# Kernel optimization log

Measured on AMD Instinct MI355X. Metric: run time of the kernel, lower is better.

Reference implementation:

```python
import jax, jax.numpy as jnp
import numpy as np

N_EMBD = 1024
N_HEADS = 16
HEAD_DIM = N_EMBD // N_HEADS


def setup_inputs() -> dict:
    key = jax.random.key(0)
    k0, k1, k2, k3, k4 = jax.random.split(key, 5)
    scale = 1.0 / np.sqrt(N_EMBD)
    x = jax.random.normal(k0, (2, 2048, N_EMBD), dtype=jnp.float32)
    # nn.Linear(n_embd, 3*n_embd): weight [3d, d], bias [3d]
    w_qkv = jax.random.normal(k1, (3 * N_EMBD, N_EMBD), dtype=jnp.float32) * scale
    b_qkv = jax.random.normal(k2, (3 * N_EMBD,), dtype=jnp.float32) * scale
    w_proj = jax.random.normal(k3, (N_EMBD, N_EMBD), dtype=jnp.float32) * scale
    b_proj = jax.random.normal(k4, (N_EMBD,), dtype=jnp.float32) * scale
    return {"x": x, "w_qkv": w_qkv, "b_qkv": b_qkv, "w_proj": w_proj, "b_proj": b_proj}


def reference(x, w_qkv, b_qkv, w_proj, b_proj):
    b, l, d = x.shape
    h, f = N_HEADS, HEAD_DIM
    qkv = x @ w_qkv.T + b_qkv                      # [b, l, 3d]
    # rearrange 'b l (c h f) -> c b h l f'
    qkv = qkv.reshape(b, l, 3, h, f)
    q = jnp.transpose(qkv[:, :, 0], (0, 2, 1, 3))  # [b, h, l, f]
    k = jnp.transpose(qkv[:, :, 1], (0, 2, 1, 3))
    v = jnp.transpose(qkv[:, :, 2], (0, 2, 1, 3))
    scores = jnp.einsum('bhqf,bhkf->bhqk', q, k) / jnp.sqrt(jnp.float32(f))
    att = jax.nn.softmax(scores, axis=-1)          # [b, h, l, l]
    y = jnp.einsum('bhqk,bhkf->bhqf', att, v)      # [b, h, l, f]
    y = jnp.transpose(y, (0, 2, 1, 3)).reshape(b, l, d)  # 'b h l f -> b l (h f)'
    return y @ w_proj.T + b_proj
```

## Files before the change

### kernel.cpp

```cpp
#include <hip/hip_runtime.h>
#include <hip/hip_bf16.h>
#include <stdint.h>


typedef unsigned short u16;
typedef __attribute__((ext_vector_type(8))) short short8;
typedef __attribute__((ext_vector_type(4))) float f32x4;

#define MFMA16(a, b, c) __builtin_amdgcn_mfma_f32_16x16x32_bf16((a), (b), (c), 0, 0, 0)

__device__ __forceinline__ u16 f2bf(float x) {
  union { float f; uint32_t u; } v; v.f = x;
  uint32_t r = v.u + 0x7FFFu + ((v.u >> 16) & 1u);
  return (u16)(r >> 16);
}

__device__ __forceinline__ float fexp2(float x) {
#if __has_builtin(__builtin_amdgcn_exp2f)
  return __builtin_amdgcn_exp2f(x);
#else
  return exp2f(x);
#endif
}

__device__ __forceinline__ uint32_t pkbf(float lo, float hi) {
  uint32_t a = __builtin_bit_cast(uint32_t, lo) + 0x8000u;
  uint32_t b = __builtin_bit_cast(uint32_t, hi) + 0x8000u;
  return __builtin_amdgcn_perm(b, a, 0x07060302u);
}

__device__ __forceinline__ void gload16(const void* g, void* l) {
  __builtin_amdgcn_global_load_lds((const __attribute__((address_space(1))) void*)g,
                                   (__attribute__((address_space(3))) void*)l, 16, 0, 0);
}

__global__ __launch_bounds__(256) void cvt_all(const float* __restrict__ x,
                                               const float* __restrict__ wq,
                                               const float* __restrict__ wp,
                                               u16* __restrict__ xb,
                                               u16* __restrict__ wqb,
                                               u16* __restrict__ wpb) {
  int i = blockIdx.x * 256 + threadIdx.x;
  const float* s; u16* d; int off;
  if (i < 1048576) { s = x; d = xb; off = i; }
  else if (i < 1835008) { s = wq; d = wqb; off = i - 1048576; }
  else { s = wp; d = wpb; off = i - 1835008; }
  float4 f = reinterpret_cast<const float4*>(s)[off];
  ushort4 o;
  o.x = f2bf(f.x); o.y = f2bf(f.y); o.z = f2bf(f.z); o.w = f2bf(f.w);
  reinterpret_cast<ushort4*>(d)[off] = o;
}

template <int EPI>
__global__ __launch_bounds__(256) void gemm_bt(const u16* __restrict__ A,
                                               const u16* __restrict__ B,
                                               const float* __restrict__ bias,
                                               u16* __restrict__ outb,
                                               float* __restrict__ outf,
                                               int M, int N, int K) {
  __shared__ u16 sA[128 * 32];
  __shared__ u16 sB[128 * 32];
  const int tid = threadIdx.x;
  const int lane = tid & 63;
  const int wid = tid >> 6;
  const int bn = blockIdx.x, bm = blockIdx.y;
  const int row0 = bm * 128, col0 = bn * 128;
  const int wr = wid >> 1, wc = wid & 1;
  const int fr = lane & 15, fq = lane >> 4;

  f32x4 acc[4][4];
  #pragma unroll
  for (int m = 0; m < 4; m++)
    #pragma unroll
    for (int n = 0; n < 4; n++)
      #pragma unroll
      for (int j = 0; j < 4; j++) acc[m][n][j] = 0.f;

  const int e1 = tid * 8;
  const int e2 = e1 + 2048;
  const int r1 = e1 >> 5, c1 = e1 & 31;
  const int r2 = e2 >> 5;
  const u16* Ap1 = A + (size_t)(row0 + r1) * K + c1;
  const u16* Ap2 = A + (size_t)(row0 + r2) * K + c1;
  const u16* Bp1 = B + (size_t)(col0 + r1) * K + c1;
  const u16* Bp2 = B + (size_t)(col0 + r2) * K + c1;

  for (int k0 = 0; k0 < K; k0 += 32) {
    __syncthreads();
    gload16(Ap1 + k0, &sA[e1]);
    gload16(Ap2 + k0, &sA[e2]);
    gload16(Bp1 + k0, &sB[e1]);
    gload16(Bp2 + k0, &sB[e2]);
    __syncthreads();
    short8 a[4], b[4];
    #pragma unroll
    for (int m = 0; m < 4; m++)
      a[m] = *(const short8*)&sA[(wr * 64 + m * 16 + fr) * 32 + fq * 8];
    #pragma unroll
    for (int n = 0; n < 4; n++)
      b[n] = *(const short8*)&sB[(wc * 64 + n * 16 + fr) * 32 + fq * 8];
    #pragma unroll
    for (int m = 0; m < 4; m++)
      #pragma unroll
      for (int n = 0; n < 4; n++)
        acc[m][n] = MFMA16(a[m], b[n], acc[m][n]);
  }

  #pragma unroll
  for (int m = 0; m < 4; m++) {
    #pragma unroll
    for (int n = 0; n < 4; n++) {
      #pragma unroll
      for (int j = 0; j < 4; j++) {
        int r = row0 + wr * 64 + m * 16 + fq * 4 + j;
        int c = col0 + wc * 64 + n * 16 + fr;
        float v = acc[m][n][j] + bias[c];
        if (EPI == 0) {
          int cc = c >> 10, d = c & 1023, h = d >> 6, f = d & 63;
          int bb = r >> 11, ll = r & 2047;
          int bhh = bb * 16 + h;
          if (cc == 0) {
            outb[((size_t)bhh * 2048 + ll) * 64 + f] = f2bf(v * 0.18033688f);
          } else if (cc == 1) {
            outb[4194304u + ((size_t)bhh * 2048 + ll) * 64 + f] = f2bf(v);
          } else {
            outb[8388608u + ((size_t)bhh * 64 + f) * 2048 + ll] = f2bf(v);
          }
        } else {
          outf[(size_t)r * N + c] = v;
        }
      }
    }
  }
}

__global__ __launch_bounds__(256, 2) void attn_kernel(const u16* __restrict__ qg,
                                                      const u16* __restrict__ kg,
                                                      const u16* __restrict__ vtg,
                                                      u16* __restrict__ y) {
  __shared__ u16 sK[2][4096];
  __shared__ u16 sVt[2][4096];
  __shared__ u16 sP[4][2048];
  const int x = blockIdx.x;
  const int bh = (x & 7) * 4 + (x >> 7);
  const int qt = (x >> 3) & 15;
  const int tid = threadIdx.x, lane = tid & 63, wid = tid >> 6;
  const int fr = lane & 15, fq = lane >> 4;
  const size_t base = (size_t)bh * 131072;
  const u16* qp = qg + base;
  const u16* kp = kg + base;
  const u16* vp = vtg + base;
  const int qrow = qt * 128 + wid * 32;

  const int c2 = tid + 256;
  const int r1 = tid >> 3, r2 = c2 >> 3;
  const int sw1 = ((tid & 7) * 8) ^ ((r1 & 7) << 3);
  const int sw2 = ((c2 & 7) * 8) ^ ((r2 & 7) << 3);
  const int ko1 = r1 * 64 + sw1, ko2 = r2 * 64 + sw2;
  const int vo1 = r1 * 2048 + sw1, vo2 = r2 * 2048 + sw2;
  const int d1 = tid * 8, d2 = c2 * 8;

  short8 qf[2][2];
  #pragma unroll
  for (int mr = 0; mr < 2; mr++)
    #pragma unroll
    for (int hh = 0; hh < 2; hh++)
      qf[mr][hh] = *(const short8*)&qp[(size_t)(qrow + mr * 16 + fr) * 64 + hh * 32 + fq * 8];

  f32x4 o[2][4];
  float lp[2] = {0.f, 0.f};
  #pragma unroll
  for (int mr = 0; mr < 2; mr++)
    #pragma unroll
    for (int ct = 0; ct < 4; ct++)
      #pragma unroll
      for (int j = 0; j < 4; j++) o[mr][ct][j] = 0.f;

  const int swr = (fr & 7) << 3;

  gload16(kp + ko1, &sK[0][d1]);
  gload16(kp + ko2, &sK[0][d2]);
  gload16(vp + vo1, &sVt[0][d1]);
  gload16(vp + vo2, &sVt[0][d2]);

  int sel = 0;
  for (int t0 = 0; t0 < 2048; t0 += 64) {
    __syncthreads();
    if (t0 + 64 < 2048) {
      const int tn = t0 + 64;
      gload16(kp + (size_t)tn * 64 + ko1, &sK[sel ^ 1][d1]);
      gload16(kp + (size_t)tn * 64 + ko2, &sK[sel ^ 1][d2]);
      gload16(vp + tn + vo1, &sVt[sel ^ 1][d1]);
      gload16(vp + tn + vo2, &sVt[sel ^ 1][d2]);
    }
    const u16* Kt = sK[sel];
    const u16* Vt = sVt[sel];
    u16* P = sP[wid];

    f32x4 st[2][4];
    #pragma unroll
    for (int mr = 0; mr < 2; mr++)
      #pragma unroll
      for (int n = 0; n < 4; n++)
        #pragma unroll
        for (int j = 0; j < 4; j++) st[mr][n][j] = 0.f;
    #pragma unroll
    for (int n = 0; n < 4; n++) {
      short8 kb0 = *(const short8*)&Kt[(n * 16 + fr) * 64 + ((fq * 8) ^ swr)];
      short8 kb1 = *(const short8*)&Kt[(n * 16 + fr) * 64 + ((32 + fq * 8) ^ swr)];
      st[0][n] = MFMA16(kb0, qf[0][0], st[0][n]);
      st[0][n] = MFMA16(kb1, qf[0][1], st[0][n]);
      st[1][n] = MFMA16(kb0, qf[1][0], st[1][n]);
      st[1][n] = MFMA16(kb1, qf[1][1], st[1][n]);
    }

    #pragma unroll
    for (int mr = 0; mr < 2; mr++) {
      const int prow = (mr * 16 + fr) * 64;
      #pragma unroll
      for (int n = 0; n < 4; n++) {
        float p0 = fexp2(st[mr][n][0]);
        float p1 = fexp2(st[mr][n][1]);
        float p2 = fexp2(st[mr][n][2]);
        float p3 = fexp2(st[mr][n][3]);
        lp[mr] += (p0 + p1) + (p2 + p3);
        uint2 w;
        w.x = pkbf(p0, p1);
        w.y = pkbf(p2, p3);
        *(uint2*)&P[prow + ((n * 16 + fq * 4) ^ swr)] = w;
      }
    }

    short8 pa[2][2];
    #pragma unroll
    for (int mr = 0; mr < 2; mr++) {
      pa[mr][0] = *(const short8*)&P[(mr * 16 + fr) * 64 + ((fq * 8) ^ swr)];
      pa[mr][1] = *(const short8*)&P[(mr * 16 + fr) * 64 + ((32 + fq * 8) ^ swr)];
    }
    #pragma unroll
    for (int ct = 0; ct < 4; ct++) {
      short8 vb0 = *(const short8*)&Vt[(ct * 16 + fr) * 64 + ((fq * 8) ^ swr)];
      short8 vb1 = *(const short8*)&Vt[(ct * 16 + fr) * 64 + ((32 + fq * 8) ^ swr)];
      #pragma unroll
      for (int mr = 0; mr < 2; mr++) {
        o[mr][ct] = MFMA16(pa[mr][0], vb0, o[mr][ct]);
        o[mr][ct] = MFMA16(pa[mr][1], vb1, o[mr][ct]);
      }
    }
    sel ^= 1;
  }

  #pragma unroll
  for (int mr = 0; mr < 2; mr++) {
    lp[mr] += __shfl_xor(lp[mr], 16);
    lp[mr] += __shfl_xor(lp[mr], 32);
  }
  const int b = bh >> 4, h = bh & 15;
  #pragma unroll
  for (int mr = 0; mr < 2; mr++) {
    #pragma unroll
    for (int j = 0; j < 4; j++) {
      int r = qrow + mr * 16 + fq * 4 + j;
      float lq = __shfl(lp[mr], fq * 4 + j);
      float inv = 1.0f / lq;
      #pragma unroll
      for (int ct = 0; ct < 4; ct++) {
        y[((size_t)(b * 2048 + r)) * 1024 + h * 64 + ct * 16 + fr] = f2bf(o[mr][ct][j] * inv);
      }
    }
  }
}

extern "C" void kernel_launch(void* const* d_in, const int* in_sizes, int n_in,
                              void* d_out, int out_size, void* d_ws, size_t ws_size,
                              hipStream_t stream) {
  const float* x = (const float*)d_in[0];
  const float* w_qkv = (const float*)d_in[1];
  const float* b_qkv = (const float*)d_in[2];
  const float* w_proj = (const float*)d_in[3];
  const float* b_proj = (const float*)d_in[4];
  float* out = (float*)d_out;

  u16* ws = (u16*)d_ws;
  u16* xb = ws;
  u16* wq = xb + 4194304;
  u16* wp = wq + 3145728;
  u16* qb = wp + 1048576;
  u16* kb = qb + 4194304;
  u16* vb = kb + 4194304;
  u16* yb = vb + 4194304;

  cvt_all<<<8192, 256, 0, stream>>>(x, w_qkv, w_proj, xb, wq, wp);

  gemm_bt<0><<<dim3(24, 32), 256, 0, stream>>>(xb, wq, b_qkv, qb, nullptr, 4096, 3072, 1024);

  attn_kernel<<<512, 256, 0, stream>>>(qb, kb, vb, yb);

  gemm_bt<1><<<dim3(8, 32), 256, 0, stream>>>(yb, wp, b_proj, nullptr, out, 4096, 1024, 1024);
}
```

Baseline: 134.7 us.

## Rewrite attention with 32x32 MFMA and register-resident P; stage V-transpose epilogue via LDS

Result: slower. 147.1 us (+9.2%).

```diff
diff --git a/kernel.cpp b/kernel.cpp
--- a/kernel.cpp
+++ b/kernel.cpp
@@ -6,8 +6,11 @@
 typedef unsigned short u16;
 typedef __attribute__((ext_vector_type(8))) short short8;
 typedef __attribute__((ext_vector_type(4))) float f32x4;
+typedef __attribute__((ext_vector_type(16))) float f32x16;
+typedef __attribute__((ext_vector_type(4))) unsigned int u32x4;
 
 #define MFMA16(a, b, c) __builtin_amdgcn_mfma_f32_16x16x32_bf16((a), (b), (c), 0, 0, 0)
+#define MFMA32(a, b, c) __builtin_amdgcn_mfma_f32_32x32x16_bf16((a), (b), (c), 0, 0, 0)
 
 __device__ __forceinline__ u16 f2bf(float x) {
   union { float f; uint32_t u; } v; v.f = x;
@@ -60,6 +63,7 @@
                                                int M, int N, int K) {
   __shared__ u16 sA[128 * 32];
   __shared__ u16 sB[128 * 32];
+  __shared__ u16 sC[EPI == 0 ? 128 * 128 : 8];
   const int tid = threadIdx.x;
   const int lane = tid & 63;
   const int wid = tid >> 6;
@@ -106,167 +110,193 @@
         acc[m][n] = MFMA16(a[m], b[n], acc[m][n]);
   }
 
-  #pragma unroll
-  for (int m = 0; m < 4; m++) {
-    #pragma unroll
-    for (int n = 0; n < 4; n++) {
-      #pragma unroll
-      for (int j = 0; j < 4; j++) {
-        int r = row0 + wr * 64 + m * 16 + fq * 4 + j;
-        int c = col0 + wc * 64 + n * 16 + fr;
-        float v = acc[m][n][j] + bias[c];
-        if (EPI == 0) {
-          int cc = c >> 10, d = c & 1023, h = d >> 6, f = d & 63;
-          int bb = r >> 11, ll = r & 2047;
-          int bhh = bb * 16 + h;
-          if (cc == 0) {
-            outb[((size_t)bhh * 2048 + ll) * 64 + f] = f2bf(v * 0.18033688f);
-          } else if (cc == 1) {
-            outb[4194304u + ((size_t)bhh * 2048 + ll) * 64 + f] = f2bf(v);
-          } else {
-            outb[8388608u + ((size_t)bhh * 64 + f) * 2048 + ll] = f2bf(v);
+  if (EPI == 0) {
+    if (bn < 16) {
+      #pragma unroll
+      for (int m = 0; m < 4; m++) {
+        #pragma unroll
+        for (int n = 0; n < 4; n++) {
+          #pragma unroll
+          for (int j = 0; j < 4; j++) {
+            int r = row0 + wr * 64 + m * 16 + fq * 4 + j;
+            int c = col0 + wc * 64 + n * 16 + fr;
+            float v = acc[m][n][j] + bias[c];
+            int d = c & 1023, h = d >> 6, f = d & 63;
+            int bb = r >> 11, ll = r & 2047;
+            int bhh = bb * 16 + h;
+            if (bn < 8) {
+              outb[((size_t)bhh * 2048 + ll) * 64 + f] = f2bf(v * 0.18033688f);
+            } else {
+              outb[4194304u + ((size_t)bhh * 2048 + ll) * 64 + f] = f2bf(v);
+            }
           }
-        } else {
-          outf[(size_t)r * N + c] = v;
         }
       }
-    }
-  }
-}
-
-__global__ __launch_bounds__(256, 2) void attn_kernel(const u16* __restrict__ qg,
+    } else {
+      #pragma unroll
+      for (int m = 0; m < 4; m++) {
+        #pragma unroll
+        for (int n = 0; n < 4; n++) {
+          int c_local = wc * 64 + n * 16 + fr;
+          int r_base = wr * 64 + m * 16 + fq * 4;
+          float bi = bias[col0 + c_local];
+          uint2 w;
+          w.x = pkbf(acc[m][n][0] + bi, acc[m][n][1] + bi);
+          w.y = pkbf(acc[m][n][2] + bi, acc[m][n][3] + bi);
+          *(uint2*)&sC[c_local * 128 + (r_base ^ ((c_local & 7) << 3))] = w;
+        }
+      }
+      __syncthreads();
+      const int h0 = (col0 - 2048) >> 6;
+      const int ll0 = row0 & 2047;
+      const int bb = row0 >> 11;
+      #pragma unroll
+      for (int it = 0; it < 8; it++) {
+        int chunk = tid + it * 256;
+        int row_c = chunk >> 4, off = chunk & 15;
+        short8 v = *(const short8*)&sC[row_c * 128 + ((off * 8) ^ ((row_c & 7) << 3))];
+        int h = h0 + (row_c >> 6), f = row_c & 63;
+        *(short8*)&outb[8388608u + ((size_t)((bb * 16 + h) * 64 + f)) * 2048 + ll0 + off * 8] = v;
+      }
+    }
+  } else {
+    #pragma unroll
+    for (int m = 0; m < 4; m++)
+      #pragma unroll
+      for (int n = 0; n < 4; n++)
+        #pragma unroll
+        for (int j = 0; j < 4; j++) {
+          int r = row0 + wr * 64 + m * 16 + fq * 4 + j;
+          int c = col0 + wc * 64 + n * 16 + fr;
+          outf[(size_t)r * N + c] = acc[m][n][j] + bias[c];
+        }
+  }
+}
+
+__device__ __forceinline__ void softpack(const f32x16& st, float& lp,
+                                         short8& paA, short8& paB) {
+  float e[16];
+  #pragma unroll
+  for (int r = 0; r < 16; r++) e[r] = fexp2(st[r]);
+  #pragma unroll
+  for (int r = 0; r < 16; r++) lp += e[r];
+  #pragma unroll
+  for (int cc = 0; cc < 2; cc++) {
+    uint32_t g0 = pkbf(e[8 * cc + 0], e[8 * cc + 1]);
+    uint32_t g1 = pkbf(e[8 * cc + 2], e[8 * cc + 3]);
+    uint32_t g2 = pkbf(e[8 * cc + 4], e[8 * cc + 5]);
+    uint32_t g3 = pkbf(e[8 * cc + 6], e[8 * cc + 7]);
+    asm volatile("v_permlane32_swap_b32 %0, %1" : "+v"(g0), "+v"(g2));
+    asm volatile("v_permlane32_swap_b32 %0, %1" : "+v"(g1), "+v"(g3));
+    u32x4 t;
+    t[0] = g0; t[1] = g1; t[2] = g2; t[3] = g3;
+    if (cc == 0) paA = __builtin_bit_cast(short8, t);
+    else paB = __builtin_bit_cast(short8, t);
+  }
+}
+
+__global__ __launch_bounds__(128, 2) void attn_kernel(const u16* __restrict__ qg,
                                                       const u16* __restrict__ kg,
                                                       const u16* __restrict__ vtg,
                                                       u16* __restrict__ y) {
   __shared__ u16 sK[2][4096];
   __shared__ u16 sVt[2][4096];
-  __shared__ u16 sP[4][2048];
+  __shared__ float sLv[2][32];
   const int x = blockIdx.x;
-  const int bh = (x & 7) * 4 + (x >> 7);
-  const int qt = (x >> 3) & 15;
-  const int tid = threadIdx.x, lane = tid & 63, wid = tid >> 6;
-  const int fr = lane & 15, fq = lane >> 4;
+  const int bh = (x & 7) * 4 + (x >> 8);
+  const int qt = (x >> 3) & 31;
+  const int tid = threadIdx.x, l = tid & 63, wid = tid >> 6;
+  const int col = l & 31, hi = l >> 5;
   const size_t base = (size_t)bh * 131072;
   const u16* qp = qg + base;
   const u16* kp = kg + base;
   const u16* vp = vtg + base;
-  const int qrow = qt * 128 + wid * 32;
-
-  const int c2 = tid + 256;
-  const int r1 = tid >> 3, r2 = c2 >> 3;
-  const int sw1 = ((tid & 7) * 8) ^ ((r1 & 7) << 3);
-  const int sw2 = ((c2 & 7) * 8) ^ ((r2 & 7) << 3);
-  const int ko1 = r1 * 64 + sw1, ko2 = r2 * 64 + sw2;
-  const int vo1 = r1 * 2048 + sw1, vo2 = r2 * 2048 + sw2;
-  const int d1 = tid * 8, d2 = c2 * 8;
-
-  short8 qf[2][2];
-  #pragma unroll
-  for (int mr = 0; mr < 2; mr++)
-    #pragma unroll
-    for (int hh = 0; hh < 2; hh++)
-      qf[mr][hh] = *(const short8*)&qp[(size_t)(qrow + mr * 16 + fr) * 64 + hh * 32 + fq * 8];
-
-  f32x4 o[2][4];
-  float lp[2] = {0.f, 0.f};
-  #pragma unroll
-  for (int mr = 0; mr < 2; mr++)
-    #pragma unroll
-    for (int ct = 0; ct < 4; ct++)
-      #pragma unroll
-      for (int j = 0; j < 4; j++) o[mr][ct][j] = 0.f;
-
-  const int swr = (fr & 7) << 3;
-
-  gload16(kp + ko1, &sK[0][d1]);
-  gload16(kp + ko2, &sK[0][d2]);
-  gload16(vp + vo1, &sVt[0][d1]);
-  gload16(vp + vo2, &sVt[0][d2]);
+  const int qrow = qt * 64 + wid * 32;
+
+  short8 qf[4];
+  #pragma unroll
+  for (int kk = 0; kk < 4; kk++)
+    qf[kk] = *(const short8*)&qp[(size_t)(qrow + col) * 64 + kk * 16 + hi * 8];
+
+  int koff[4], voff[4], dst[4];
+  #pragma unroll
+  for (int j = 0; j < 4; j++) {
+    int c = tid + j * 128;
+    int row = c >> 3, slot = c & 7;
+    int swc = (slot * 8) ^ ((row & 7) << 3);
+    koff[j] = row * 64 + swc;
+    voff[j] = row * 2048 + swc;
+    dst[j] = c * 8;
+  }
+
+  f32x16 o0, o1;
+  float lp = 0.f;
+  #pragma unroll
+  for (int r = 0; r < 16; r++) { o0[r] = 0.f; o1[r] = 0.f; }
+
+  const int rsw = (col & 7) << 3;
+
+  #pragma unroll
+  for (int j = 0; j < 4; j++) {
+    gload16(kp + koff[j], &sK[0][dst[j]]);
+    gload16(vp + voff[j], &sVt[0][dst[j]]);
+  }
 
   int sel = 0;
   for (int t0 = 0; t0 < 2048; t0 += 64) {
     __syncthreads();
     if (t0 + 64 < 2048) {
       const int tn = t0 + 64;
-      gload16(kp + (size_t)tn * 64 + ko1, &sK[sel ^ 1][d1]);
-      gload16(kp + (size_t)tn * 64 + ko2, &sK[sel ^ 1][d2]);
-      gload16(vp + tn + vo1, &sVt[sel ^ 1][d1]);
-      gload16(vp + tn + vo2, &sVt[sel ^ 1][d2]);
+      #pragma unroll
+      for (int j = 0; j < 4; j++) {
+        gload16(kp + (size_t)tn * 64 + koff[j], &sK[sel ^ 1][dst[j]]);
+        gload16(vp + tn + voff[j], &sVt[sel ^ 1][dst[j]]);
+      }
     }
     const u16* Kt = sK[sel];
     const u16* Vt = sVt[sel];
-    u16* P = sP[wid];
-
-    f32x4 st[2][4];
-    #pragma unroll
-    for (int mr = 0; mr < 2; mr++)
-      #pragma unroll
-      for (int n = 0; n < 4; n++)
-        #pragma unroll
-        for (int j = 0; j < 4; j++) st[mr][n][j] = 0.f;
-    #pragma unroll
-    for (int n = 0; n < 4; n++) {
-      short8 kb0 = *(const short8*)&Kt[(n * 16 + fr) * 64 + ((fq * 8) ^ swr)];
-      short8 kb1 = *(const short8*)&Kt[(n * 16 + fr) * 64 + ((32 + fq * 8) ^ swr)];
-      st[0][n] = MFMA16(kb0, qf[0][0], st[0][n]);
-      st[0][n] = MFMA16(kb1, qf[0][1], st[0][n]);
-      st[1][n] = MFMA16(kb0, qf[1][0], st[1][n]);
-      st[1][n] = MFMA16(kb1, qf[1][1], st[1][n]);
-    }
-
-    #pragma unroll
-    for (int mr = 0; mr < 2; mr++) {
-      const int prow = (mr * 16 + fr) * 64;
-      #pragma unroll
-      for (int n = 0; n < 4; n++) {
-        float p0 = fexp2(st[mr][n][0]);
-        float p1 = fexp2(st[mr][n][1]);
-        float p2 = fexp2(st[mr][n][2]);
-        float p3 = fexp2(st[mr][n][3]);
-        lp[mr] += (p0 + p1) + (p2 + p3);
-        uint2 w;
-        w.x = pkbf(p0, p1);
-        w.y = pkbf(p2, p3);
-        *(uint2*)&P[prow + ((n * 16 + fq * 4) ^ swr)] = w;
-      }
-    }
-
-    short8 pa[2][2];
-    #pragma unroll
-    for (int mr = 0; mr < 2; mr++) {
-      pa[mr][0] = *(const short8*)&P[(mr * 16 + fr) * 64 + ((fq * 8) ^ swr)];
-      pa[mr][1] = *(const short8*)&P[(mr * 16 + fr) * 64 + ((32 + fq * 8) ^ swr)];
-    }
-    #pragma unroll
-    for (int ct = 0; ct < 4; ct++) {
-      short8 vb0 = *(const short8*)&Vt[(ct * 16 + fr) * 64 + ((fq * 8) ^ swr)];
-      short8 vb1 = *(const short8*)&Vt[(ct * 16 + fr) * 64 + ((32 + fq * 8) ^ swr)];
-      #pragma unroll
-      for (int mr = 0; mr < 2; mr++) {
-        o[mr][ct] = MFMA16(pa[mr][0], vb0, o[mr][ct]);
-        o[mr][ct] = MFMA16(pa[mr][1], vb1, o[mr][ct]);
-      }
-    }
+
+    f32x16 st0, st1;
+    #pragma unroll
+    for (int r = 0; r < 16; r++) { st0[r] = 0.f; st1[r] = 0.f; }
+    __builtin_amdgcn_s_setprio(1);
+    #pragma unroll
+    for (int kk = 0; kk < 4; kk++) {
+      short8 kb0 = *(const short8*)&Kt[(col) * 64 + ((kk * 16 + hi * 8) ^ rsw)];
+      short8 kb1 = *(const short8*)&Kt[(32 + col) * 64 + ((kk * 16 + hi * 8) ^ rsw)];
+      st0 = MFMA32(kb0, qf[kk], st0);
+      st1 = MFMA32(kb1, qf[kk], st1);
+    }
+    __builtin_amdgcn_s_setprio(0);
+
+    short8 pa[4];
+    softpack(st0, lp, pa[0], pa[1]);
+    softpack(st1, lp, pa[2], pa[3]);
+
+    __builtin_amdgcn_s_setprio(1);
+    #pragma unroll
+    for (int c = 0; c < 4; c++) {
+      short8 vb0 = *(const short8*)&Vt[(col) * 64 + ((c * 16 + hi * 8) ^ rsw)];
+      short8 vb1 = *(const short8*)&Vt[(32 + col) * 64 + ((c * 16 + hi * 8) ^ rsw)];
+      o0 = MFMA32(pa[c], vb0, o0);
+      o1 = MFMA32(pa[c], vb1, o1);
+    }
+    __builtin_amdgcn_s_setprio(0);
     sel ^= 1;
   }
 
-  #pragma unroll
-  for (int mr = 0; mr < 2; mr++) {
-    lp[mr] += __shfl_xor(lp[mr], 16);
-    lp[mr] += __shfl_xor(lp[mr], 32);
-  }
-  const int b = bh >> 4, h = bh & 15;
-  #pragma unroll
-  for (int mr = 0; mr < 2; mr++) {
-    #pragma unroll
-    for (int j = 0; j < 4; j++) {
-      int r = qrow + mr * 16 + fq * 4 + j;
-      float lq = __shfl(lp[mr], fq * 4 + j);
-      float inv = 1.0f / lq;
-      #pragma unroll
-      for (int ct = 0; ct < 4; ct++) {
-        y[((size_t)(b * 2048 + r)) * 1024 + h * 64 + ct * 16 + fr] = f2bf(o[mr][ct][j] * inv);
-      }
+  float lsum = lp + __shfl_xor(lp, 32);
+  float linv = 1.0f / lsum;
+  if (l < 32) sLv[wid][col] = linv;
+  const int b = bh >> 4, hh = bh & 15;
+  #pragma unroll
+  for (int fvt = 0; fvt < 2; fvt++) {
+    #pragma unroll
+    for (int r = 0; r < 16; r++) {
+      int q = (r & 3) + 8 * (r >> 2) + 4 * hi;
+      float li = sLv[wid][q];
+      float v = (fvt == 0 ? o0[r] : o1[r]) * li;
+      y[((size_t)(b * 2048 + qrow + q)) * 1024 + hh * 64 + fvt * 32 + col] = f2bf(v);
     }
   }
 }
@@ -294,7 +324,7 @@
 
   gemm_bt<0><<<dim3(24, 32), 256, 0, stream>>>(xb, wq, b_qkv, qb, nullptr, 4096, 3072, 1024);
 
-  attn_kernel<<<512, 256, 0, stream>>>(qb, kb, vb, yb);
+  attn_kernel<<<1024, 128, 0, stream>>>(qb, kb, vb, yb);
 
   gemm_bt<1><<<dim3(8, 32), 256, 0, stream>>>(yb, wp, b_proj, nullptr, out, 4096, 1024, 1024);
 }
```
